# Performance work log

Measured on AMD Instinct MI355X. Metric: run time of the kernel, lower is better.

## Reference

```python
import jax, jax.numpy as jnp
import numpy as np
from jax import lax

B_SZ, SEQ, D_MODEL = 8, 2048, 1024
N_LAYER = 2
D_INNER = 2 * D_MODEL          # expand=2
D_STATE = 16
D_CONV = 4
DT_RANK = D_MODEL // 16        # ceil(1024/16)=64
EPS = 1e-5


def setup_inputs() -> dict:
    key = jax.random.key(0)
    ks = jax.random.split(key, 8)
    f = lambda k, shp, sc: jax.random.normal(k, shp, jnp.float32) * sc
    A_log = jnp.tile(jnp.log(jnp.arange(1, D_STATE + 1, dtype=jnp.float32)),
                     (N_LAYER, D_INNER, 1))  # S4D-real init, [L, d_inner, d_state]
    return {
        "x": f(ks[0], (B_SZ, SEQ, D_MODEL), 1.0),
        "in_proj_w": f(ks[1], (N_LAYER, 2 * D_INNER, D_MODEL), 0.02),
        "conv_w": f(ks[2], (N_LAYER, D_INNER, D_CONV), 0.2),
        "conv_b": jnp.zeros((N_LAYER, D_INNER), jnp.float32),
        "x_proj_w": f(ks[3], (N_LAYER, DT_RANK + 2 * D_STATE, D_INNER), 0.02),
        "dt_proj_w": f(ks[4], (N_LAYER, D_INNER, DT_RANK), 0.1),
        "dt_proj_b": f(ks[5], (N_LAYER, D_INNER), 0.5) - 4.0,  # softplus -> small dt
        "A_log": A_log,
        "D_param": jnp.ones((N_LAYER, D_INNER), jnp.float32),
        "out_proj_w": f(ks[6], (N_LAYER, D_MODEL, D_INNER), 0.02),
        "norm_w": jnp.ones((N_LAYER, D_MODEL), jnp.float32),
        "norm_b": jnp.zeros((N_LAYER, D_MODEL), jnp.float32),
    }


def _layer_norm(x, w, b):
    mu = jnp.mean(x, axis=-1, keepdims=True)
    var = jnp.mean(jnp.square(x - mu), axis=-1, keepdims=True)
    return (x - mu) * lax.rsqrt(var + EPS) * w + b


def _causal_dw_conv(x, w, b):
    # x: [B, Lq, d_inner], w: [d_inner, d_conv] depthwise causal conv
    xp = jnp.pad(x, ((0, 0), (D_CONV - 1, 0), (0, 0)))
    L = x.shape[1]
    y = b
    for k in range(D_CONV):
        y = y + xp[:, k:k + L, :] * w[:, k]
    return y


def _selective_scan(u, dt, Bm, Cm, A, Dp):
    # u, dt: [B, Lq, d_inner]; Bm, Cm: [B, Lq, d_state]; A: [d_inner, d_state]
    def step(h, inp):
        ut, dtt, Bt, Ct = inp                         # [B,di],[B,di],[B,ds],[B,ds]
        dA = jnp.exp(dtt[..., None] * A)              # [B, di, ds]
        h = dA * h + (dtt * ut)[..., None] * Bt[:, None, :]
        y = jnp.einsum('bds,bs->bd', h, Ct)
        return h, y

    h0 = jnp.zeros((u.shape[0], D_INNER, D_STATE), u.dtype)
    xs = (u.transpose(1, 0, 2), dt.transpose(1, 0, 2),
          Bm.transpose(1, 0, 2), Cm.transpose(1, 0, 2))
    _, ys = lax.scan(step, h0, xs)                    # ys: [Lq, B, di]
    return ys.transpose(1, 0, 2) + u * Dp


def _mamba(x, in_w, cw, cb, xpw, dtw, dtb, A_log, Dp, ow):
    xz = jnp.einsum('bld,ed->ble', x, in_w)           # [B, L, 2*d_inner]
    xi, z = jnp.split(xz, 2, axis=-1)
    xc = jax.nn.silu(_causal_dw_conv(xi, cw, cb))     # [B, L, d_inner]
    xdbl = jnp.einsum('bld,ed->ble', xc, xpw)         # [B, L, dt_rank+2*d_state]
    dt_low = xdbl[..., :DT_RANK]
    Bm = xdbl[..., DT_RANK:DT_RANK + D_STATE]
    Cm = xdbl[..., DT_RANK + D_STATE:]
    dt = jax.nn.softplus(jnp.einsum('blr,dr->bld', dt_low, dtw) + dtb)
    A = -jnp.exp(A_log)                               # [d_inner, d_state]
    y = _selective_scan(xc, dt, Bm, Cm, A, Dp)
    y = y * jax.nn.silu(z)
    return jnp.einsum('ble,de->bld', y, ow)           # [B, L, d_model]


def reference(x, in_proj_w, conv_w, conv_b, x_proj_w, dt_proj_w, dt_proj_b,
              A_log, D_param, out_proj_w, norm_w, norm_b):
    residual = None
    for l in range(N_LAYER):
        residual = x if residual is None else x + residual
        h = _layer_norm(residual, norm_w[l], norm_b[l])
        x = _mamba(h, in_proj_w[l], conv_w[l], conv_b[l], x_proj_w[l],
                   dt_proj_w[l], dt_proj_b[l], A_log[l], D_param[l], out_proj_w[l])
    # NOTE: source forward returns x without applying norm_f
    return x
```

## Files before the change

### kernel.cpp

```cpp
#include <hip/hip_runtime.h>
#include <cstddef>
#include <cstdint>

#define SEQB   8
#define SEQL   2048
#define DMODEL 1024
#define DINNER 2048
#define DSTATE 16
#define NC     32
#define TC     64
#define TT     8

typedef __attribute__((ext_vector_type(4))) float f32x4;
typedef __attribute__((ext_vector_type(8))) short bf16x8;
typedef unsigned int u32;
typedef const __attribute__((address_space(1))) u32* gas_ptr;
typedef __attribute__((address_space(3))) u32* las_ptr;

__device__ __forceinline__ void gld16(const void* g, void* l){
  __builtin_amdgcn_global_load_lds((gas_ptr)g, (las_ptr)l, 16, 0, 0);
}

__device__ __forceinline__ float siluf(float x){ return x / (1.f + __expf(-x)); }
__device__ __forceinline__ float softplusf(float x){ return (x > 20.f) ? x : log1pf(__expf(x)); }

__device__ __forceinline__ unsigned short f2bf_rne(float f){
  unsigned int u = __float_as_uint(f);
  u += 0x7FFFu + ((u>>16)&1u);
  return (unsigned short)(u>>16);
}
__device__ __forceinline__ void split_bf(float f, unsigned short& h, unsigned short& l){
  unsigned short hs = f2bf_rne(f);
  float hf = __uint_as_float(((unsigned int)hs)<<16);
  h = hs;
  l = f2bf_rne(f - hf);
}

__global__ __launch_bounds__(256)
void wsplit2(const float* __restrict__ src, unsigned short* __restrict__ dst,
             int K, int k4shift)
{
  int idx = blockIdx.x*256 + threadIdx.x;
  int r  = idx >> k4shift;
  int c4 = idx & ((1<<k4shift)-1);
  float4 v = ((const float4*)src)[idx];
  unsigned short h,l; short4 h4, l4;
  split_bf(v.x,h,l); h4.x=(short)h; l4.x=(short)l;
  split_bf(v.y,h,l); h4.y=(short)h; l4.y=(short)l;
  split_bf(v.z,h,l); h4.z=(short)h; l4.z=(short)l;
  split_bf(v.w,h,l); h4.w=(short)h; l4.w=(short)l;
  size_t ro = (size_t)r*2*K;
  *(short4*)&dst[ro + (c4<<2)]     = h4;
  *(short4*)&dst[ro + K + (c4<<2)] = l4;
}

__global__ __launch_bounds__(256)
void wsplit_og(const float* __restrict__ src, unsigned short* __restrict__ dst)
{
  int idx = blockIdx.x*256 + threadIdx.x;
  int r  = idx >> 9;
  int c4 = idx & 511;
  int layer = r >> 10, rr = r & 1023;
  float4 v = ((const float4*)src)[idx];
  unsigned short h,l; short4 h4, l4;
  split_bf(v.x,h,l); h4.x=(short)h; l4.x=(short)l;
  split_bf(v.y,h,l); h4.y=(short)h; l4.y=(short)l;
  split_bf(v.z,h,l); h4.z=(short)h; l4.z=(short)l;
  split_bf(v.w,h,l); h4.w=(short)h; l4.w=(short)l;
  int col = c4 << 2;
  int g = col >> 8, j = col & 255;
  size_t base = (size_t)layer*1024*4096 + (size_t)rr*4096 + g*512 + j;
  *(short4*)&dst[base]       = h4;
  *(short4*)&dst[base + 256] = l4;
}

__global__ __launch_bounds__(256)
void ln_split2(const float* __restrict__ a, const float* __restrict__ res,
               const float* __restrict__ w, const float* __restrict__ bias,
               unsigned short* __restrict__ Hs)
{
  int row = blockIdx.x;
  size_t off = (size_t)row * DMODEL;
  float4 v = ((const float4*)(a + off))[threadIdx.x];
  if (res){
    float4 u = ((const float4*)(res + off))[threadIdx.x];
    v.x += u.x; v.y += u.y; v.z += u.z; v.w += u.w;
  }
  float s  = v.x + v.y + v.z + v.w;
  float s2 = fmaf(v.x,v.x, fmaf(v.y,v.y, fmaf(v.z,v.z, v.w*v.w)));
  #pragma unroll
  for (int o=32;o>0;o>>=1){ s += __shfl_down(s,o,64); s2 += __shfl_down(s2,o,64); }
  __shared__ float red[8];
  int lane = threadIdx.x & 63, wid = threadIdx.x >> 6;
  if (lane==0){ red[wid]=s; red[4+wid]=s2; }
  __syncthreads();
  s  = red[0]+red[1]+red[2]+red[3];
  s2 = red[4]+red[5]+red[6]+red[7];
  float mu  = s * (1.f/DMODEL);
  float var = s2 * (1.f/DMODEL) - mu*mu;
  float rstd = rsqrtf(var + 1e-5f);
  float4 wv = ((const float4*)w)[threadIdx.x];
  float4 bv = ((const float4*)bias)[threadIdx.x];
  float4 o4;
  o4.x = (v.x-mu)*rstd*wv.x + bv.x;
  o4.y = (v.y-mu)*rstd*wv.y + bv.y;
  o4.z = (v.z-mu)*rstd*wv.z + bv.z;
  o4.w = (v.w-mu)*rstd*wv.w + bv.w;
  unsigned short h,l; short4 h4, l4;
  split_bf(o4.x,h,l); h4.x=(short)h; l4.x=(short)l;
  split_bf(o4.y,h,l); h4.y=(short)h; l4.y=(short)l;
  split_bf(o4.z,h,l); h4.z=(short)h; l4.z=(short)l;
  split_bf(o4.w,h,l); h4.w=(short)h; l4.w=(short)l;
  size_t ro = (size_t)row*2048;
  int c = threadIdx.x<<2;
  *(short4*)&Hs[ro + c]        = h4;
  *(short4*)&Hs[ro + 1024 + c] = l4;
}

__global__ __launch_bounds__(256)
void mgemm_in(const unsigned short* __restrict__ A,
              const unsigned short* __restrict__ B,
              float* __restrict__ XI, float* __restrict__ ZB)
{
  __shared__ __align__(16) unsigned short As[128*64];
  __shared__ __align__(16) unsigned short Bs[128*64];
  const int t = threadIdx.x;
  const int mbase = blockIdx.y << 7, nbase = blockIdx.x << 7;

  const int lane = t & 63, w = t >> 6;
  const int wr = w >> 1, wc = w & 1;
  const int l16 = lane & 15, kq = lane >> 4;

  const int sr8 = lane >> 3, sl8 = lane & 7;
  const unsigned short* pA[4]; const unsigned short* pB[4];
  unsigned short* dA[4]; unsigned short* dB[4];
  #pragma unroll
  for (int c=0;c<4;c++){
    int row = c*32 + w*8 + sr8;
    int col = (sl8 ^ (row & 7)) << 3;
    pA[c] = A + (size_t)(mbase+row)*2048 + col;
    pB[c] = B + (size_t)(nbase+row)*2048 + col;
    dA[c] = &As[row*64 + sl8*8];
    dB[c] = &Bs[row*64 + sl8*8];
  }

  f32x4 acc[4][4];
  #pragma unroll
  for (int i=0;i<4;i++)
    #pragma unroll
    for (int j=0;j<4;j++) acc[i][j] = (f32x4){0.f,0.f,0.f,0.f};

  #pragma unroll
  for (int kb=0; kb<3; kb++){
    const int ao = (kb==2) ? 1024 : 0;
    const int bo = (kb==1) ? 1024 : 0;
    for (int kk=0; kk<1024; kk+=64){
      #pragma unroll
      for (int c=0;c<4;c++){
        gld16(pA[c] + ao + kk, dA[c]);
        gld16(pB[c] + bo + kk, dB[c]);
      }
      __syncthreads();
      #pragma unroll
      for (int ks=0; ks<2; ks++){
        const int kcol = kq + ks*4;
        bf16x8 af[4];
        #pragma unroll
        for (int mf=0; mf<4; mf++){
          int ra = wr*64 + mf*16 + l16;
          af[mf] = *(const bf16x8*)&As[ra*64 + ((kcol ^ (ra&7))<<3)];
        }
        #pragma unroll
        for (int nf=0; nf<4; nf++){
          int rb = wc*64 + nf*16 + l16;
          bf16x8 bfr = *(const bf16x8*)&Bs[rb*64 + ((kcol ^ (rb&7))<<3)];
          #pragma unroll
          for (int mf=0; mf<4; mf++)
            acc[mf][nf] = __builtin_amdgcn_mfma_f32_16x16x32_bf16(af[mf], bfr, acc[mf][nf], 0,0,0);
        }
      }
      __syncthreads();
    }
  }

  float* Cd = (nbase < 2048) ? XI : ZB;
  const int cb = (nbase < 2048) ? nbase : (nbase - 2048);
  #pragma unroll
  for (int mf=0; mf<4; mf++){
    int r0 = mbase + wr*64 + mf*16 + kq*4;
    #pragma unroll
    for (int nf=0; nf<4; nf++){
      int c = cb + wc*64 + nf*16 + l16;
      #pragma unroll
      for (int r=0;r<4;r++)
        Cd[(size_t)(r0+r)*2048 + c] = acc[mf][nf][r];
    }
  }
}

__global__ __launch_bounds__(256)
void mgemm_out3(const unsigned short* __restrict__ A,
                const unsigned short* __restrict__ B,
                float* __restrict__ C)
{
  __shared__ __align__(16) unsigned short As[128*64];
  __shared__ __align__(16) unsigned short Bs[128*64];
  const int t = threadIdx.x;
  const int mbase = blockIdx.y << 7, nbase = blockIdx.x << 7;

  const int lane = t & 63, w = t >> 6;
  const int wr = w >> 1, wc = w & 1;
  const int l16 = lane & 15, kq = lane >> 4;

  const int sr8 = lane >> 3, sl8 = lane & 7;
  const unsigned short* pA[4]; const unsigned short* pB[4];
  unsigned short* dA[4]; unsigned short* dB[4];
  #pragma unroll
  for (int c=0;c<4;c++){
    int row = c*32 + w*8 + sr8;
    int col = (sl8 ^ (row & 7)) << 3;
    pA[c] = A + (size_t)(mbase+row)*4096 + col;
    pB[c] = B + (size_t)(nbase+row)*4096 + col;
    dA[c] = &As[row*64 + sl8*8];
    dB[c] = &Bs[row*64 + sl8*8];
  }

  f32x4 acc[4][4];
  #pragma unroll
  for (int i=0;i<4;i++)
    #pragma unroll
    for (int j=0;j<4;j++) acc[i][j] = (f32x4){0.f,0.f,0.f,0.f};

  #pragma unroll
  for (int kb=0; kb<3; kb++){
    const int pa_ = (kb==2) ? 256 : 0;
    const int pb_ = (kb==1) ? 256 : 0;
    for (int v=0; v<2048; v+=64){
      const int gso = ((v>>8)<<9) + (v & 255);
      #pragma unroll
      for (int c=0;c<4;c++){
        gld16(pA[c] + gso + pa_, dA[c]);
        gld16(pB[c] + gso + pb_, dB[c]);
      }
      __syncthreads();
      #pragma unroll
      for (int ks=0; ks<2; ks++){
        const int kcol = kq + ks*4;
        bf16x8 af[4];
        #pragma unroll
        for (int mf=0; mf<4; mf++){
          int ra = wr*64 + mf*16 + l16;
          af[mf] = *(const bf16x8*)&As[ra*64 + ((kcol ^ (ra&7))<<3)];
        }
        #pragma unroll
        for (int nf=0; nf<4; nf++){
          int rb = wc*64 + nf*16 + l16;
          bf16x8 bfr = *(const bf16x8*)&Bs[rb*64 + ((kcol ^ (rb&7))<<3)];
          #pragma unroll
          for (int mf=0; mf<4; mf++)
            acc[mf][nf] = __builtin_amdgcn_mfma_f32_16x16x32_bf16(af[mf], bfr, acc[mf][nf], 0,0,0);
        }
      }
      __syncthreads();
    }
  }

  #pragma unroll
  for (int mf=0; mf<4; mf++){
    int r0 = mbase + wr*64 + mf*16 + kq*4;
    #pragma unroll
    for (int nf=0; nf<4; nf++){
      int c = nbase + wc*64 + nf*16 + l16;
      #pragma unroll
      for (int r=0;r<4;r++)
        C[(size_t)(r0+r)*1024 + c] = acc[mf][nf][r];
    }
  }
}

__global__ __launch_bounds__(256)
void xproj_pair(const unsigned short* __restrict__ A,
                const unsigned short* __restrict__ W2,
                float* __restrict__ XD)
{
  __shared__ __align__(16) unsigned short As_[32*32];
  __shared__ __align__(16) unsigned short Bs_[96*32];
  const int t = threadIdx.x;
  const int mbase = blockIdx.x << 5;
  const int lane = t & 63, w = t >> 6;
  const int mf = w & 1, nc0 = (w >> 1) * 48;
  const int l16 = lane & 15, kq = lane >> 4;

  const bool isA0 = (w < 2);
  const int rr = lane >> 2, sl = lane & 3;
  const int r0_ = (isA0 ? 16*w : 16*(w-2)) + rr;
  const int sw0 = ((sl ^ ((r0_>>1)&3)) << 3);
  const unsigned short* base0 = isA0 ? (A + (size_t)(mbase+r0_)*4096 + sw0)
                                     : (W2 + (size_t)r0_*4096 + sw0);
  unsigned short* dst0 = isA0 ? (As_ + w*512 + lane*8)
                              : (Bs_ + (w-2)*512 + lane*8);
  const int r1_ = 16*(w+2) + rr;
  const int sw1 = ((sl ^ ((r1_>>1)&3)) << 3);
  const unsigned short* base1 = W2 + (size_t)r1_*4096 + sw1;
  unsigned short* dst1 = Bs_ + (w+2)*512 + lane*8;

  f32x4 acc[3];
  #pragma unroll
  for (int j=0;j<3;j++) acc[j] = (f32x4){0.f,0.f,0.f,0.f};

  #pragma unroll
  for (int kb=0; kb<3; kb++){
    const int ao = (kb==2) ? 2048 : 0;
    const int bo = (kb==1) ? 2048 : 0;
    const int off0 = isA0 ? ao : bo;
    for (int v=0; v<2048; v+=32){
      gld16(base0 + off0 + v, dst0);
      gld16(base1 + bo + v, dst1);
      __syncthreads();
      int ra = mf*16 + l16;
      bf16x8 a = *(const bf16x8*)&As_[ra*32 + ((kq ^ ((ra>>1)&3))<<3)];
      #pragma unroll
      for (int nf=0; nf<3; nf++){
        int rb = nc0 + nf*16 + l16;
        bf16x8 b = *(const bf16x8*)&Bs_[rb*32 + ((kq ^ ((rb>>1)&3))<<3)];
        acc[nf] = __builtin_amdgcn_mfma_f32_16x16x32_bf16(a, b, acc[nf], 0,0,0);
      }
      __syncthreads();
    }
  }
  #pragma unroll
  for (int nf=0; nf<3; nf++){
    int c = nc0 + nf*16 + l16;
    int r0s = mbase + mf*16 + kq*4;
    #pragma unroll
    for (int r=0;r<4;r++)
      XD[(size_t)(r0s+r)*96 + c] = acc[nf][r];
  }
}

__global__ __launch_bounds__(256)
void gemm_dt(const float* __restrict__ A, int lda,
             const float* __restrict__ B, int ldb,
             float* __restrict__ C, int ldc,
             int K, const float* __restrict__ ebias)
{
  __shared__ float As[16][132];
  __shared__ float Bs[16][132];
  int tid = threadIdx.x;
  int tx = tid & 15, ty = tid >> 4;
  int mbase = blockIdx.y << 7;
  int nbase = blockIdx.x << 7;
  float acc[8][8];
  #pragma unroll
  for (int i=0;i<8;i++)
    #pragma unroll
    for (int j=0;j<8;j++) acc[i][j]=0.f;

  for (int k0=0;k0<K;k0+=16){
    #pragma unroll
    for (int it=0; it<2; it++){
      int idx = tid + (it<<8);
      int row = idx >> 2;
      int kq  = (idx & 3) << 2;
      float4 va = *(const float4*)(A + (size_t)(mbase+row)*lda + k0 + kq);
      As[kq+0][row]=va.x; As[kq+1][row]=va.y; As[kq+2][row]=va.z; As[kq+3][row]=va.w;
      float4 vb = *(const float4*)(B + (size_t)(nbase+row)*ldb + k0 + kq);
      Bs[kq+0][row]=vb.x; Bs[kq+1][row]=vb.y; Bs[kq+2][row]=vb.z; Bs[kq+3][row]=vb.w;
    }
    __syncthreads();
    #pragma unroll
    for (int k=0;k<16;k++){
      float a[8], bb[8];
      *(float4*)&a[0]  = *(const float4*)&As[k][ty<<2];
      *(float4*)&a[4]  = *(const float4*)&As[k][64+(ty<<2)];
      *(float4*)&bb[0] = *(const float4*)&Bs[k][tx<<2];
      *(float4*)&bb[4] = *(const float4*)&Bs[k][64+(tx<<2)];
      #pragma unroll
      for (int i=0;i<8;i++)
        #pragma unroll
        for (int j=0;j<8;j++)
          acc[i][j] = fmaf(a[i], bb[j], acc[i][j]);
    }
    __syncthreads();
  }

  int n0 = nbase + (tx<<2);
  int n1 = n0 + 64;
  float4 eb0 = *(const float4*)(ebias + n0);
  float4 eb1 = *(const float4*)(ebias + n1);
  #pragma unroll
  for (int i=0;i<8;i++){
    int mrow = mbase + ((i<4) ? ((ty<<2)+i) : (64 + (ty<<2) + (i-4)));
    float4 c0 = make_float4(acc[i][0],acc[i][1],acc[i][2],acc[i][3]);
    float4 c1 = make_float4(acc[i][4],acc[i][5],acc[i][6],acc[i][7]);
    c0.x = softplusf(c0.x+eb0.x); c0.y = softplusf(c0.y+eb0.y);
    c0.z = softplusf(c0.z+eb0.z); c0.w = softplusf(c0.w+eb0.w);
    c1.x = softplusf(c1.x+eb1.x); c1.y = softplusf(c1.y+eb1.y);
    c1.z = softplusf(c1.z+eb1.z); c1.w = softplusf(c1.w+eb1.w);
    *(float4*)(C + (size_t)mrow*ldc + n0) = c0;
    *(float4*)(C + (size_t)mrow*ldc + n1) = c1;
  }
}

__global__ __launch_bounds__(256)
void conv_silu_kernel(const float* __restrict__ xi, const float* __restrict__ cw,
                      const float* __restrict__ cb, unsigned short* __restrict__ u2)
{
  const int row = blockIdx.x;
  const int d0 = threadIdx.x << 3;
  const int tt = row & (SEQL-1);

  float wk[4][8];
  {
    const float4* cw4 = (const float4*)(cw + (size_t)d0*4);
    #pragma unroll
    for (int j=0;j<8;j++){
      float4 wj = cw4[j];
      wk[0][j]=wj.x; wk[1][j]=wj.y; wk[2][j]=wj.z; wk[3][j]=wj.w;
    }
  }
  float bias[8];
  *(float4*)&bias[0] = *(const float4*)(cb + d0);
  *(float4*)&bias[4] = *(const float4*)(cb + d0 + 4);

  const float* base = xi + (size_t)row*DINNER + d0;
  float r0[8], r1[8], r2[8], r3[8];
#define LD8(dst, p) { *(float4*)&dst[0] = ((const float4*)(p))[0]; \
                      *(float4*)&dst[4] = ((const float4*)(p))[1]; }
  LD8(r0, base);
  if (tt>=1){ LD8(r1, base-DINNER); }   else { for(int j=0;j<8;j++) r1[j]=0.f; }
  if (tt>=2){ LD8(r2, base-2*DINNER); } else { for(int j=0;j<8;j++) r2[j]=0.f; }
  if (tt>=3){ LD8(r3, base-3*DINNER); } else { for(int j=0;j<8;j++) r3[j]=0.f; }
#undef LD8

  unsigned short h8[8], l8[8];
  #pragma unroll
  for (int j=0;j<8;j++){
    float y = fmaf(r0[j], wk[3][j], fmaf(r1[j], wk[2][j],
              fmaf(r2[j], wk[1][j], fmaf(r3[j], wk[0][j], bias[j]))));
    float uv = siluf(y);
    split_bf(uv, h8[j], l8[j]);
  }
  unsigned short* outp = u2 + (size_t)row*4096 + d0;
  *(uint4*)outp          = *(const uint4*)h8;
  *(uint4*)(outp + 2048) = *(const uint4*)l8;
}

template<int PASS>
__global__ __launch_bounds__(256)
void scan_chunk(const unsigned short* __restrict__ u2, float* __restrict__ dty,
                const float* __restrict__ xdbl, const float* __restrict__ zb,
                const float* __restrict__ A_log, const float* __restrict__ Dp,
                float* __restrict__ hfin, float* __restrict__ sumdt)
{
  __shared__ __align__(16) float Tdt[2][TT][256];
  __shared__ __align__(16) float Tu [2][TT][256];
  __shared__ __align__(16) float Tz [(PASS==3)?2:1][(PASS==3)?TT:1][(PASS==3)?256:4];
  __shared__ __align__(16) float Tbc[2][TT][32];

  const int tid = threadIdx.x;
  const int idx = blockIdx.x*256 + tid;
  const int d = idx & (DINNER-1);
  const int g = idx >> 11;
  const int cck = g & (NC-1);
  const int bb = g >> 5;
  const int wv = tid >> 6, ln = tid & 63;
  const int dbase = (blockIdx.x << 8) & (DINNER-1);

  float A2[16];
  {
    const float* al = A_log + (size_t)d*DSTATE;
    #pragma unroll
    for (int s=0;s<16;s++) A2[s] = -expf(al[s]) * 1.44269504f;
  }
  float h[16];
  if (PASS == 1){
    #pragma unroll
    for (int s=0;s<16;s++) h[s] = 0.f;
  } else {
    const float* hp = hfin + ((size_t)g*DINNER + d)*16;
    #pragma unroll
    for (int s=0;s<16;s+=4) *(float4*)&h[s] = *(const float4*)(hp + s);
  }
  const float Dv = (PASS==3) ? Dp[d] : 0.f;

  const size_t row0 = (size_t)bb*SEQL + (size_t)cck*TC;

#define STAGE(buf, T0) do { \
    _Pragma("unroll") \
    for (int q=0;q<2;q++){ \
      int r = q*4 + wv; \
      size_t rowi = row0 + (T0) + r; \
      gld16(dty + rowi*2048 + dbase + ln*4, &Tdt[buf][r][0]); \
      const unsigned short* us = u2 + rowi*4096 + \
          ((ln < 32) ? (dbase + ln*8) : (2048 + dbase + (ln-32)*8)); \
      gld16(us, &Tu[buf][r][0]); \
      if (PASS==3) gld16(zb + rowi*2048 + dbase + ln*4, &Tz[buf][r][0]); \
    } \
    if (wv == 3){ \
      gld16(xdbl + (row0 + (T0) + (ln>>3))*96 + 64 + (ln&7)*4, &Tbc[buf][0][0]); \
    } \
  } while(0)

  STAGE(0, 0);
  asm volatile("s_waitcnt vmcnt(0)" ::: "memory");
  __builtin_amdgcn_s_barrier();
  __builtin_amdgcn_sched_barrier(0);

  float sdt = 0.f;

  for (int t0 = 0; t0 < TC; t0 += TT){
    const int cur = (t0 >> 3) & 1, nxt = cur ^ 1;
    const bool hasNext = (t0 + TT < TC);
    if (hasNext) STAGE(nxt, t0 + TT);

    if (hasNext){
      if (PASS==3){
        if (wv==3) asm volatile("s_waitcnt vmcnt(7)" ::: "memory");
        else       asm volatile("s_waitcnt vmcnt(6)" ::: "memory");
      } else {
        if (wv==3) asm volatile("s_waitcnt vmcnt(5)" ::: "memory");
        else       asm volatile("s_waitcnt vmcnt(4)" ::: "memory");
      }
    } else {
      asm volatile("s_waitcnt vmcnt(0)" ::: "memory");
    }
    __builtin_amdgcn_s_barrier();
    __builtin_amdgcn_sched_barrier(0);

    #pragma unroll
    for (int tt=0; tt<TT; tt++){
      float dtc = Tdt[cur][tt][tid];
      const unsigned short* tur = (const unsigned short*)&Tu[cur][tt][0];
      float uc = __uint_as_float((u32)tur[tid] << 16)
               + __uint_as_float((u32)tur[256+tid] << 16);
      float Bv[16], Cv[16];
      #pragma unroll
      for (int q=0;q<4;q++) *(float4*)&Bv[q*4] = *(const float4*)&Tbc[cur][tt][q*4];
      if (PASS==3){
        #pragma unroll
        for (int q=0;q<4;q++) *(float4*)&Cv[q*4] = *(const float4*)&Tbc[cur][tt][16+q*4];
      }
      if (PASS==1) sdt += dtc;
      float du = dtc*uc;
      float y = 0.f;
      #pragma unroll
      for (int s=0;s<16;s++){
        float dA = exp2f(dtc*A2[s]);
        h[s] = fmaf(dA, h[s], du*Bv[s]);
        if (PASS==3) y = fmaf(h[s], Cv[s], y);
      }
      if (PASS==3){
        float zc = Tz[cur][tt][tid];
        y = fmaf(uc, Dv, y);
        float gv = y * siluf(zc);
        unsigned short gh, gl;
        split_bf(gv, gh, gl);
        Tdt[cur][tt][tid] = __uint_as_float((u32)gh | ((u32)gl << 16));
      }
    }

    if (PASS==3) asm volatile("s_waitcnt lgkmcnt(0)" ::: "memory");
    __builtin_amdgcn_s_barrier();
    __builtin_amdgcn_sched_barrier(0);

    if (PASS==3){
      #pragma unroll
      for (int q=0;q<2;q++){
        int r = q*4 + wv;
        size_t rowi = row0 + t0 + r;
        const u32* T = (const u32*)&Tdt[cur][r][0];
        int o0 = ln*4;
        u32 vals[4];
        if (ln < 32){
          #pragma unroll
          for (int k=0;k<4;k++){
            int i2 = (o0+k)*2;
            vals[k] = (T[i2] & 0xFFFFu) | (T[i2+1] << 16);
          }
        } else {
          #pragma unroll
          for (int k=0;k<4;k++){
            int i2 = (o0+k-128)*2;
            vals[k] = (T[i2] >> 16) | (T[i2+1] & 0xFFFF0000u);
          }
        }
        *(float4*)(dty + rowi*2048 + dbase + o0) = *(const float4*)vals;
      }
    }
  }
#undef STAGE

  if (PASS==1){
    float* hp = hfin + ((size_t)g*DINNER + d)*16;
    #pragma unroll
    for (int s=0;s<16;s+=4) *(float4*)(hp + s) = *(const float4*)&h[s];
    sumdt[(size_t)g*DINNER + d] = sdt;
  }
}

__global__ __launch_bounds__(256)
void scan_prop(const float* __restrict__ A_log, float* __restrict__ hfin,
               const float* __restrict__ sumdt)
{
  int idx = blockIdx.x*256 + threadIdx.x;
  int s = idx & 15;
  int d = (idx >> 4) & (DINNER-1);
  int b = idx >> 15;
  float A2 = -expf(A_log[(size_t)d*DSTATE + s]) * 1.44269504f;
  float H = 0.f;
  size_t hbase = ((size_t)b*NC*DINNER + d)*16 + s;
  size_t sbase = (size_t)b*NC*DINNER + d;
  for (int c=0;c<NC;c++){
    float P   = exp2f(A2 * sumdt[sbase + (size_t)c*DINNER]);
    float tmp = hfin[hbase + (size_t)c*DINNER*16];
    hfin[hbase + (size_t)c*DINNER*16] = H;
    H = fmaf(P, H, tmp);
  }
}

extern "C" void kernel_launch(void* const* d_in, const int* in_sizes, int n_in,
                              void* d_out, int out_size, void* d_ws, size_t ws_size,
                              hipStream_t stream)
{
  const float* x    = (const float*)d_in[0];
  const float* in_w = (const float*)d_in[1];
  const float* cw   = (const float*)d_in[2];
  const float* cb   = (const float*)d_in[3];
  const float* xpw  = (const float*)d_in[4];
  const float* dtw  = (const float*)d_in[5];
  const float* dtb  = (const float*)d_in[6];
  const float* A_log= (const float*)d_in[7];
  const float* Dp   = (const float*)d_in[8];
  const float* ow   = (const float*)d_in[9];
  const float* nw   = (const float*)d_in[10];
  const float* nb   = (const float*)d_in[11];
  float* outF = (float*)d_out;

  const size_t fixedB = 33554432ULL + 16777216ULL + 1572864ULL;
  const size_t perB   = 58720256ULL;
  int NB = 4;
  while (NB > 1 && fixedB + (size_t)NB*perB > ws_size) NB >>= 1;
  const int Mc = NB * SEQL;
  const int nchunk = SEQB / NB;

  unsigned short* INW2  = (unsigned short*)d_ws;
  unsigned short* OUTWG = INW2 + (size_t)2*4096*2048;
  unsigned short* XPW2  = OUTWG + (size_t)2*1024*4096;
  char* dyn = (char*)(XPW2 + (size_t)2*96*4096);

  unsigned short* SH = (unsigned short*)dyn;
  float* XD = (float*)dyn;
  float* HF = (float*)(dyn + (size_t)Mc*384);
  float* SD = (float*)(dyn + (size_t)Mc*2432);
  float* XI = (float*)(dyn + (size_t)Mc*4096);
  float* ZB = XI + (size_t)Mc*2048;
  unsigned short* U2 = (unsigned short*)(ZB + (size_t)Mc*2048);

  wsplit2<<<8192, 256, 0, stream>>>(in_w, INW2, 1024, 8);
  wsplit2<<<384,  256, 0, stream>>>(xpw,  XPW2, 2048, 9);
  wsplit_og<<<4096, 256, 0, stream>>>(ow, OUTWG);

  for (int c = 0; c < nchunk; ++c){
    const size_t rowoff = (size_t)c * Mc;
    const float* xrows = x + rowoff * DMODEL;
    float* X1 = outF + rowoff * DMODEL;

    for (int l = 0; l < 2; ++l){
      const float* Al = A_log + (size_t)l*DINNER*DSTATE;

      ln_split2<<<Mc, 256, 0, stream>>>(
          (l==0) ? xrows : X1, (l==0) ? nullptr : xrows,
          nw + (size_t)l*DMODEL, nb + (size_t)l*DMODEL, SH);

      mgemm_in<<<dim3(32, Mc/128), 256, 0, stream>>>(
          SH, INW2 + (size_t)l*4096*2048, XI, ZB);

      conv_silu_kernel<<<Mc, 256, 0, stream>>>(
          XI, cw + (size_t)l*DINNER*4, cb + (size_t)l*DINNER, U2);

      xproj_pair<<<Mc/32, 256, 0, stream>>>(
          U2, XPW2 + (size_t)l*96*4096, XD);

      gemm_dt<<<dim3(16, Mc/128), 256, 0, stream>>>(
          XD, 96, dtw + (size_t)l*DINNER*64, 64, XI, DINNER, 64,
          dtb + (size_t)l*DINNER);

      scan_chunk<1><<<NB*NC*8, 256, 0, stream>>>(
          U2, XI, XD, ZB, Al, Dp + (size_t)l*DINNER, HF, SD);
      scan_prop<<<NB*128, 256, 0, stream>>>(Al, HF, SD);
      scan_chunk<3><<<NB*NC*8, 256, 0, stream>>>(
          U2, XI, XD, ZB, Al, Dp + (size_t)l*DINNER, HF, SD);

      mgemm_out3<<<dim3(8, Mc/128), 256, 0, stream>>>(
          (const unsigned short*)XI, OUTWG + (size_t)l*1024*4096, X1);
    }
  }
}
```

Measured before the change: 3.654 ms.

## Load hi and lo bf16 split parts in one tile for 3-term GEMMs

The three split-bf16 GEMMs (in_proj, out_proj, x_proj) previously ran three separate K passes (hi*hi, hi*lo, lo*hi), each reloading tiles from global memory. Now each LDS tile holds both the hi and lo halves for a 32-wide K slice. All three MFMA products are issued from the same loaded fragments, which cuts global loads and syncs by roughly a third. The cost is more MFMAs per sync and more live fragment registers. x_proj is also reorganised into a single unified shared buffer.

After: 3.307 ms. 9.5% less time.

```diff
diff --git a/kernel.cpp b/kernel.cpp
--- a/kernel.cpp
+++ b/kernel.cpp
@@ -137,9 +137,10 @@
   #pragma unroll
   for (int c=0;c<4;c++){
     int row = c*32 + w*8 + sr8;
-    int col = (sl8 ^ (row & 7)) << 3;
-    pA[c] = A + (size_t)(mbase+row)*2048 + col;
-    pB[c] = B + (size_t)(nbase+row)*2048 + col;
+    int ss  = sl8 ^ (row & 7);
+    int colb = (ss < 4) ? (ss<<3) : (1024 + ((ss-4)<<3));
+    pA[c] = A + (size_t)(mbase+row)*2048 + colb;
+    pB[c] = B + (size_t)(nbase+row)*2048 + colb;
     dA[c] = &As[row*64 + sl8*8];
     dB[c] = &Bs[row*64 + sl8*8];
   }
@@ -150,37 +151,33 @@
     #pragma unroll
     for (int j=0;j<4;j++) acc[i][j] = (f32x4){0.f,0.f,0.f,0.f};
 
-  #pragma unroll
-  for (int kb=0; kb<3; kb++){
-    const int ao = (kb==2) ? 1024 : 0;
-    const int bo = (kb==1) ? 1024 : 0;
-    for (int kk=0; kk<1024; kk+=64){
-      #pragma unroll
-      for (int c=0;c<4;c++){
-        gld16(pA[c] + ao + kk, dA[c]);
-        gld16(pB[c] + bo + kk, dB[c]);
+  for (int k0=0; k0<1024; k0+=32){
+    #pragma unroll
+    for (int c=0;c<4;c++){
+      gld16(pA[c] + k0, dA[c]);
+      gld16(pB[c] + k0, dB[c]);
+    }
+    __syncthreads();
+    bf16x8 ah[4], al[4];
+    #pragma unroll
+    for (int mf=0; mf<4; mf++){
+      int ra = wr*64 + mf*16 + l16;
+      ah[mf] = *(const bf16x8*)&As[ra*64 + (( kq      ^ (ra&7))<<3)];
+      al[mf] = *(const bf16x8*)&As[ra*64 + (((kq+4)   ^ (ra&7))<<3)];
+    }
+    #pragma unroll
+    for (int nf=0; nf<4; nf++){
+      int rb = wc*64 + nf*16 + l16;
+      bf16x8 bh = *(const bf16x8*)&Bs[rb*64 + (( kq    ^ (rb&7))<<3)];
+      bf16x8 bl = *(const bf16x8*)&Bs[rb*64 + (((kq+4) ^ (rb&7))<<3)];
+      #pragma unroll
+      for (int mf=0; mf<4; mf++){
+        acc[mf][nf] = __builtin_amdgcn_mfma_f32_16x16x32_bf16(ah[mf], bh, acc[mf][nf], 0,0,0);
+        acc[mf][nf] = __builtin_amdgcn_mfma_f32_16x16x32_bf16(ah[mf], bl, acc[mf][nf], 0,0,0);
+        acc[mf][nf] = __builtin_amdgcn_mfma_f32_16x16x32_bf16(al[mf], bh, acc[mf][nf], 0,0,0);
       }
-      __syncthreads();
-      #pragma unroll
-      for (int ks=0; ks<2; ks++){
-        const int kcol = kq + ks*4;
-        bf16x8 af[4];
-        #pragma unroll
-        for (int mf=0; mf<4; mf++){
-          int ra = wr*64 + mf*16 + l16;
-          af[mf] = *(const bf16x8*)&As[ra*64 + ((kcol ^ (ra&7))<<3)];
-        }
-        #pragma unroll
-        for (int nf=0; nf<4; nf++){
-          int rb = wc*64 + nf*16 + l16;
-          bf16x8 bfr = *(const bf16x8*)&Bs[rb*64 + ((kcol ^ (rb&7))<<3)];
-          #pragma unroll
-          for (int mf=0; mf<4; mf++)
-            acc[mf][nf] = __builtin_amdgcn_mfma_f32_16x16x32_bf16(af[mf], bfr, acc[mf][nf], 0,0,0);
-        }
-      }
-      __syncthreads();
-    }
+    }
+    __syncthreads();
   }
 
   float* Cd = (nbase < 2048) ? XI : ZB;
@@ -218,9 +215,10 @@
   #pragma unroll
   for (int c=0;c<4;c++){
     int row = c*32 + w*8 + sr8;
-    int col = (sl8 ^ (row & 7)) << 3;
-    pA[c] = A + (size_t)(mbase+row)*4096 + col;
-    pB[c] = B + (size_t)(nbase+row)*4096 + col;
+    int ss  = sl8 ^ (row & 7);
+    int pofs = (ss < 4) ? (ss<<3) : (256 + ((ss-4)<<3));
+    pA[c] = A + (size_t)(mbase+row)*4096 + pofs;
+    pB[c] = B + (size_t)(nbase+row)*4096 + pofs;
     dA[c] = &As[row*64 + sl8*8];
     dB[c] = &Bs[row*64 + sl8*8];
   }
@@ -231,38 +229,34 @@
     #pragma unroll
     for (int j=0;j<4;j++) acc[i][j] = (f32x4){0.f,0.f,0.f,0.f};
 
-  #pragma unroll
-  for (int kb=0; kb<3; kb++){
-    const int pa_ = (kb==2) ? 256 : 0;
-    const int pb_ = (kb==1) ? 256 : 0;
-    for (int v=0; v<2048; v+=64){
-      const int gso = ((v>>8)<<9) + (v & 255);
-      #pragma unroll
-      for (int c=0;c<4;c++){
-        gld16(pA[c] + gso + pa_, dA[c]);
-        gld16(pB[c] + gso + pb_, dB[c]);
+  for (int k0=0; k0<2048; k0+=32){
+    const int gso = ((k0>>8)<<9) + (k0 & 255);
+    #pragma unroll
+    for (int c=0;c<4;c++){
+      gld16(pA[c] + gso, dA[c]);
+      gld16(pB[c] + gso, dB[c]);
+    }
+    __syncthreads();
+    bf16x8 ah[4], al[4];
+    #pragma unroll
+    for (int mf=0; mf<4; mf++){
+      int ra = wr*64 + mf*16 + l16;
+      ah[mf] = *(const bf16x8*)&As[ra*64 + (( kq      ^ (ra&7))<<3)];
+      al[mf] = *(const bf16x8*)&As[ra*64 + (((kq+4)   ^ (ra&7))<<3)];
+    }
+    #pragma unroll
+    for (int nf=0; nf<4; nf++){
+      int rb = wc*64 + nf*16 + l16;
+      bf16x8 bh = *(const bf16x8*)&Bs[rb*64 + (( kq    ^ (rb&7))<<3)];
+      bf16x8 bl = *(const bf16x8*)&Bs[rb*64 + (((kq+4) ^ (rb&7))<<3)];
+      #pragma unroll
+      for (int mf=0; mf<4; mf++){
+        acc[mf][nf] = __builtin_amdgcn_mfma_f32_16x16x32_bf16(ah[mf], bh, acc[mf][nf], 0,0,0);
+        acc[mf][nf] = __builtin_amdgcn_mfma_f32_16x16x32_bf16(ah[mf], bl, acc[mf][nf], 0,0,0);
+        acc[mf][nf] = __builtin_amdgcn_mfma_f32_16x16x32_bf16(al[mf], bh, acc[mf][nf], 0,0,0);
       }
-      __syncthreads();
-      #pragma unroll
-      for (int ks=0; ks<2; ks++){
-        const int kcol = kq + ks*4;
-        bf16x8 af[4];
-        #pragma unroll
-        for (int mf=0; mf<4; mf++){
-          int ra = wr*64 + mf*16 + l16;
-          af[mf] = *(const bf16x8*)&As[ra*64 + ((kcol ^ (ra&7))<<3)];
-        }
-        #pragma unroll
-        for (int nf=0; nf<4; nf++){
-          int rb = wc*64 + nf*16 + l16;
-          bf16x8 bfr = *(const bf16x8*)&Bs[rb*64 + ((kcol ^ (rb&7))<<3)];
-          #pragma unroll
-          for (int mf=0; mf<4; mf++)
-            acc[mf][nf] = __builtin_amdgcn_mfma_f32_16x16x32_bf16(af[mf], bfr, acc[mf][nf], 0,0,0);
-        }
-      }
-      __syncthreads();
-    }
+    }
+    __syncthreads();
   }
 
   #pragma unroll
@@ -283,50 +277,46 @@
                 const unsigned short* __restrict__ W2,
                 float* __restrict__ XD)
 {
-  __shared__ __align__(16) unsigned short As_[32*32];
-  __shared__ __align__(16) unsigned short Bs_[96*32];
+  __shared__ __align__(16) unsigned short S[128*64];
   const int t = threadIdx.x;
   const int mbase = blockIdx.x << 5;
   const int lane = t & 63, w = t >> 6;
   const int mf = w & 1, nc0 = (w >> 1) * 48;
   const int l16 = lane & 15, kq = lane >> 4;
 
-  const bool isA0 = (w < 2);
-  const int rr = lane >> 2, sl = lane & 3;
-  const int r0_ = (isA0 ? 16*w : 16*(w-2)) + rr;
-  const int sw0 = ((sl ^ ((r0_>>1)&3)) << 3);
-  const unsigned short* base0 = isA0 ? (A + (size_t)(mbase+r0_)*4096 + sw0)
-                                     : (W2 + (size_t)r0_*4096 + sw0);
-  unsigned short* dst0 = isA0 ? (As_ + w*512 + lane*8)
-                              : (Bs_ + (w-2)*512 + lane*8);
-  const int r1_ = 16*(w+2) + rr;
-  const int sw1 = ((sl ^ ((r1_>>1)&3)) << 3);
-  const unsigned short* base1 = W2 + (size_t)r1_*4096 + sw1;
-  unsigned short* dst1 = Bs_ + (w+2)*512 + lane*8;
+  const unsigned short* ps[4]; unsigned short* ds[4];
+  #pragma unroll
+  for (int c=0;c<4;c++){
+    int idx = c*256 + t;
+    int row = idx >> 3, sl8 = idx & 7;
+    int ss  = sl8 ^ (row & 7);
+    int colb = (ss < 4) ? (ss<<3) : (2048 + ((ss-4)<<3));
+    ps[c] = (row < 32) ? (A + (size_t)(mbase+row)*4096 + colb)
+                       : (W2 + (size_t)(row-32)*4096 + colb);
+    ds[c] = &S[row*64 + sl8*8];
+  }
 
   f32x4 acc[3];
   #pragma unroll
   for (int j=0;j<3;j++) acc[j] = (f32x4){0.f,0.f,0.f,0.f};
 
-  #pragma unroll
-  for (int kb=0; kb<3; kb++){
-    const int ao = (kb==2) ? 2048 : 0;
-    const int bo = (kb==1) ? 2048 : 0;
-    const int off0 = isA0 ? ao : bo;
-    for (int v=0; v<2048; v+=32){
-      gld16(base0 + off0 + v, dst0);
-      gld16(base1 + bo + v, dst1);
-      __syncthreads();
-      int ra = mf*16 + l16;
-      bf16x8 a = *(const bf16x8*)&As_[ra*32 + ((kq ^ ((ra>>1)&3))<<3)];
-      #pragma unroll
-      for (int nf=0; nf<3; nf++){
-        int rb = nc0 + nf*16 + l16;
-        bf16x8 b = *(const bf16x8*)&Bs_[rb*32 + ((kq ^ ((rb>>1)&3))<<3)];
-        acc[nf] = __builtin_amdgcn_mfma_f32_16x16x32_bf16(a, b, acc[nf], 0,0,0);
-      }
-      __syncthreads();
-    }
+  for (int k0=0; k0<2048; k0+=32){
+    #pragma unroll
+    for (int c=0;c<4;c++) gld16(ps[c] + k0, ds[c]);
+    __syncthreads();
+    int ra = mf*16 + l16;
+    bf16x8 ah = *(const bf16x8*)&S[ra*64 + (( kq    ^ (ra&7))<<3)];
+    bf16x8 al = *(const bf16x8*)&S[ra*64 + (((kq+4) ^ (ra&7))<<3)];
+    #pragma unroll
+    for (int nf=0; nf<3; nf++){
+      int rb = 32 + nc0 + nf*16 + l16;
+      bf16x8 bh = *(const bf16x8*)&S[rb*64 + (( kq    ^ (rb&7))<<3)];
+      bf16x8 bl = *(const bf16x8*)&S[rb*64 + (((kq+4) ^ (rb&7))<<3)];
+      acc[nf] = __builtin_amdgcn_mfma_f32_16x16x32_bf16(ah, bh, acc[nf], 0,0,0);
+      acc[nf] = __builtin_amdgcn_mfma_f32_16x16x32_bf16(ah, bl, acc[nf], 0,0,0);
+      acc[nf] = __builtin_amdgcn_mfma_f32_16x16x32_bf16(al, bh, acc[nf], 0,0,0);
+    }
+    __syncthreads();
   }
   #pragma unroll
   for (int nf=0; nf<3; nf++){
```
